# Optimization experiments

Measured on AMD Instinct MI355X. Metric: run time of the kernel, lower is better.

Reference implementation:

```python
import jax, jax.numpy as jnp
import numpy as np

B, N, C, H = 64, 300, 256, 8  # batch, patches (img 1x300, patch 1x1), dim, heads
STD = 0.02


def setup_inputs() -> dict:
    key = jax.random.key(0)
    ks = jax.random.split(key, 6)
    return {
        "x": jax.random.normal(ks[0], (B, N, C), jnp.float32),
        "Wqk": jax.random.normal(ks[1], (2 * C, C), jnp.float32) * STD,
        "Wv": jax.random.normal(ks[2], (C, C), jnp.float32) * STD,
        "Wpos": jax.random.normal(ks[3], (H, 3), jnp.float32) * STD,
        "bpos": jnp.zeros((H,), jnp.float32),
        "Wproj": jax.random.normal(ks[4], (C, C), jnp.float32) * STD,
        "bproj": jnp.zeros((C,), jnp.float32),
        "gating": jnp.ones((H,), jnp.float32),
    }


def _rel_indices(n):
    d = (jnp.arange(n)[None, :] - jnp.arange(n)[:, None]).astype(jnp.float32)
    return jnp.stack([d, jnp.zeros_like(d), d * d], axis=-1)  # [N, N, 3]


def reference(x, Wqk, Wv, Wpos, bpos, Wproj, bproj, gating):
    Bb, Nn, Cc = x.shape
    Hh = gating.shape[0]
    hd = Cc // Hh
    scale = hd ** -0.5

    qk = (x @ Wqk.T).reshape(Bb, Nn, 2, Hh, hd)
    q = qk[:, :, 0].transpose(0, 2, 1, 3)  # [B,H,N,hd]
    k = qk[:, :, 1].transpose(0, 2, 1, 3)

    patch_score = jax.nn.softmax(jnp.einsum('bhnd,bhmd->bhnm', q, k) * scale, axis=-1)

    rel = _rel_indices(Nn)                               # [N,N,3]
    pos_score = (rel @ Wpos.T + bpos).transpose(2, 0, 1)  # [H,N,N]
    pos_score = jax.nn.softmax(pos_score, axis=-1)

    g = jax.nn.sigmoid(gating)[None, :, None, None]       # [1,H,1,1]
    attn = (1.0 - g) * patch_score + g * pos_score[None]
    attn = attn / attn.sum(axis=-1, keepdims=True)

    v = (x @ Wv.T).reshape(Bb, Nn, Hh, hd).transpose(0, 2, 1, 3)  # [B,H,N,hd]
    out = jnp.einsum('bhnm,bhmd->bhnd', attn, v)
    out = out.transpose(0, 2, 1, 3).reshape(Bb, Nn, Cc)
    return out @ Wproj.T + bproj
```

## Files before the change

kernel.cpp:

```cpp
#include <hip/hip_runtime.h>


#define NSEQ 300
#define HEADS 8
#define HD 32

typedef short v8s __attribute__((ext_vector_type(8)));
typedef float v4f __attribute__((ext_vector_type(4)));
typedef unsigned int v4u __attribute__((ext_vector_type(4)));

__device__ __forceinline__ ushort f2bf(float f) {
    unsigned u = __float_as_uint(f);
    u = (u + 0x7FFFu + ((u >> 16) & 1u)) >> 16;
    return (ushort)u;
}

__device__ __forceinline__ unsigned pk2bf(float a, float b) {
    unsigned ua = __float_as_uint(a), ub = __float_as_uint(b);
    ua += 0x7FFFu + ((ua >> 16) & 1u);
    ub += 0x7FFFu + ((ub >> 16) & 1u);
    return __builtin_amdgcn_perm(ub, ua, 0x07060302);
}

__device__ __forceinline__ unsigned cvtpk(float a, float b) {
    unsigned r;
    asm("v_cvt_pk_bf16_f32 %0, %1, %2" : "=v"(r) : "v"(a), "v"(b));
    return r;
}

__device__ __forceinline__ float fexp2(float x) {
    float r; asm("v_exp_f32 %0, %1" : "=v"(r) : "v"(x)); return r;
}

__device__ __forceinline__ void gl_lds16(const ushort* g, ushort* l) {
    __builtin_amdgcn_global_load_lds(
        (const __attribute__((address_space(1))) void*)g,
        (__attribute__((address_space(3))) void*)l, 16, 0, 0);
}

__global__ __launch_bounds__(256) void prep_kernel(
    const float* __restrict__ x,
    const float* __restrict__ Wqk, const float* __restrict__ Wv,
    const float* __restrict__ Wproj, const float* __restrict__ Wpos,
    const float* __restrict__ bpos, const float* __restrict__ gating,
    ushort* __restrict__ x_bf, ushort* __restrict__ Wf,
    ushort* __restrict__ wproj_t, ushort* __restrict__ gpos)
{
    int bid = blockIdx.x, tid = threadIdx.x;
    if (bid < 2432) {
        int idx = bid * 256 + tid;
        int c8 = idx & 31;
        int mrow = idx >> 5;
        unsigned b = (unsigned)mrow / 304u;
        int r = mrow - (int)b * 304;
        v4u pk = {0u, 0u, 0u, 0u};
        if (r < 300) {
            const float* src = x + ((size_t)b * 300 + r) * 256 + c8 * 8;
            float4 f0 = *(const float4*)src;
            float4 f1 = *(const float4*)(src + 4);
            pk = (v4u){pk2bf(f0.x, f0.y), pk2bf(f0.z, f0.w),
                       pk2bf(f1.x, f1.y), pk2bf(f1.z, f1.w)};
        }
        *(v4u*)&x_bf[(size_t)mrow * 256 + c8 * 8] = pk;
        return;
    }
    if (bid < 3040) {
        int sub = bid - 2432;
        int h = sub / 76;
        int i = (sub % 76) * 4 + (tid >> 6);
        int lane = tid & 63;
        ushort* gr = gpos + ((size_t)h * 304 + i) * 304;
        if (i >= NSEQ) {
#pragma unroll
            for (int t = 0; t < 5; ++t) {
                int j = lane + 64 * t;
                if (j < 304) gr[j] = 0;
            }
            return;
        }
        float w0 = Wpos[h * 3 + 0], w2 = Wpos[h * 3 + 2], bb = bpos[h];
        float g = 1.f / (1.f + __expf(-gating[h]));
        float sv[5]; float m2 = -1e30f;
#pragma unroll
        for (int t = 0; t < 5; ++t) {
            int j = lane + 64 * t;
            float d = (float)(j - i);
            float lg = fmaf(w2, d * d, fmaf(w0, d, bb));
            sv[t] = (j < NSEQ) ? lg : -1e30f;
            m2 = fmaxf(m2, sv[t]);
        }
#pragma unroll
        for (int off = 32; off > 0; off >>= 1) m2 = fmaxf(m2, __shfl_xor(m2, off));
        float sum = 0.f;
#pragma unroll
        for (int t = 0; t < 5; ++t) { sv[t] = __expf(sv[t] - m2); sum += sv[t]; }
#pragma unroll
        for (int off = 32; off > 0; off >>= 1) sum += __shfl_xor(sum, off);
        float gi = g / sum;
#pragma unroll
        for (int t = 0; t < 5; ++t) {
            int j = lane + 64 * t;
            if (j < NSEQ) gr[j] = f2bf(sv[t] * gi);
            else if (j < 304) gr[j] = 0;
        }
        return;
    }
    if (bid < 3136) {
        int idx = (bid - 3040) * 256 + tid;
        int c = idx & 7;
        int t = idx >> 3;
        int hk = t / 96;
        int wc = t - hk * 96;
        int h = hk >> 2, kt = hk & 3;
        const float* src;
        if (wc < 32)      src = Wqk + (size_t)(h * 32 + wc) * 256;
        else if (wc < 64) src = Wqk + (size_t)(256 + h * 32 + (wc - 32)) * 256;
        else              src = Wv + (size_t)(h * 32 + (wc - 64)) * 256;
        src += kt * 64 + c * 8;
        float4 f0 = *(const float4*)src;
        float4 f1 = *(const float4*)(src + 4);
        v4u pk = {pk2bf(f0.x, f0.y), pk2bf(f0.z, f0.w),
                  pk2bf(f1.x, f1.y), pk2bf(f1.z, f1.w)};
        *(v4u*)&Wf[((size_t)(hk * 96 + wc)) * 64 + ((c ^ (wc & 7)) * 8)] = pk;
        return;
    }
    {
        int idx = (bid - 3136) * 256 + tid;
        int m = idx >> 5, ck = idx & 31;
        const float* src = Wproj + (size_t)m * 256 + ck * 8;
        int rt = m >> 7, rr = m & 127, kt = ck >> 3, c = ck & 7;
        float4 f0 = *(const float4*)src;
        float4 f1 = *(const float4*)(src + 4);
        v4u pk = {pk2bf(f0.x, f0.y), pk2bf(f0.z, f0.w),
                  pk2bf(f1.x, f1.y), pk2bf(f1.z, f1.w)};
        *(v4u*)&wproj_t[((size_t)(rt * 4 + kt) * 128 + rr) * 64 + ((c ^ (rr & 7)) * 8)] = pk;
    }
}

__global__ __launch_bounds__(256, 2) void fused_qkv_attn(
    const ushort* __restrict__ x_bf, const ushort* __restrict__ Wf,
    const ushort* __restrict__ gpos, const float* __restrict__ gating,
    ushort* __restrict__ ot)
{
    __shared__ ushort smem[34816];
    ushort* Xs = smem;
    ushort* Wsh = smem + 19456;
    ushort* Qs = smem;
    ushort* Ks = smem + 12160;
    ushort* Vt = smem + 24320;

    int bid = blockIdx.x, b = bid & 63, h = bid >> 6;
    int tid = threadIdx.x, wave = tid >> 6, lane = tid & 63, li = lane & 15, qd = lane >> 4;

    const ushort* xbb = x_bf + (size_t)b * 304 * 256;
    const ushort* wfh = Wf + (size_t)h * 4 * 6144;

    v4f acc[5][6];
#pragma unroll
    for (int i = 0; i < 5; ++i)
#pragma unroll
        for (int j = 0; j < 6; ++j) acc[i][j] = (v4f){0.f, 0.f, 0.f, 0.f};

    for (int kt = 0; kt < 4; ++kt) {
#pragma unroll
        for (int s = 0; s < 3; ++s) {
            int c = s * 256 + tid;
            gl_lds16(wfh + (size_t)kt * 6144 + c * 8, Wsh + c * 8);
        }
#pragma unroll
        for (int s = 0; s < 9; ++s) {
            int cch = s * 256 + tid;
            int r = cch >> 3, sl = cch & 7;
            gl_lds16(xbb + (size_t)r * 256 + kt * 64 + ((sl ^ (r & 7)) * 8),
                     Xs + cch * 8);
        }
        if (tid < 128) {
            int cch = 2304 + tid;
            int r = cch >> 3, sl = cch & 7;
            gl_lds16(xbb + (size_t)r * 256 + kt * 64 + ((sl ^ (r & 7)) * 8),
                     Xs + cch * 8);
        }
        __syncthreads();
#pragma unroll
        for (int kc = 0; kc < 64; kc += 32) {
            int cb = (kc >> 3) + qd;
            int cs = cb ^ (li & 7);
            v8s bw[6];
#pragma unroll
            for (int ct = 0; ct < 6; ++ct)
                bw[ct] = *(const v8s*)&Wsh[(ct * 16 + li) * 64 + cs * 8];
#pragma unroll
            for (int i = 0; i < 5; ++i) {
                int rt = wave + i * 4;
                if (rt < 19) {
                    v8s ax = *(const v8s*)&Xs[(rt * 16 + li) * 64 + cs * 8];
#pragma unroll
                    for (int ct = 0; ct < 6; ++ct)
                        acc[i][ct] = __builtin_amdgcn_mfma_f32_16x16x32_bf16(bw[ct], ax, acc[i][ct], 0, 0, 0);
                }
            }
        }
        __syncthreads();
    }

    const float QSC = 0.25503486063f;
#pragma unroll
    for (int i = 0; i < 5; ++i) {
        int rt = wave + i * 4;
        if (rt < 19) {
            int row = rt * 16 + li;
#pragma unroll
            for (int ct = 0; ct < 2; ++ct) {
                uint2 wq = {cvtpk(acc[i][ct][0] * QSC, acc[i][ct][1] * QSC),
                            cvtpk(acc[i][ct][2] * QSC, acc[i][ct][3] * QSC)};
                *(uint2*)&Qs[row * 40 + ct * 16 + qd * 4] = wq;
            }
#pragma unroll
            for (int ct = 2; ct < 4; ++ct) {
                uint2 wk = {cvtpk(acc[i][ct][0], acc[i][ct][1]),
                            cvtpk(acc[i][ct][2], acc[i][ct][3])};
                *(uint2*)&Ks[row * 40 + (ct - 2) * 16 + qd * 4] = wk;
            }
#pragma unroll
            for (int ct = 4; ct < 6; ++ct)
#pragma unroll
                for (int r = 0; r < 4; ++r)
                    Vt[((ct - 4) * 16 + qd * 4 + r) * 328 + row] = f2bf(acc[i][ct][r]);
        }
    }
    float g = 1.f / (1.f + __expf(-gating[h]));
    float omg = 1.f - g;
    __syncthreads();

    const ushort* ksp0 = &Ks[li * 40 + qd * 8];
    const ushort* vtp0 = &Vt[li * 328 + qd * 4];
    const ushort* vtp1 = &Vt[(16 + li) * 328 + qd * 4];
    const v4f z4 = {0.f, 0.f, 0.f, 0.f};

    for (int rg = wave; rg < 19; rg += 4) {
        int i0 = rg * 16;
        v8s bq = *(const v8s*)&Qs[(i0 + li) * 40 + qd * 8];
        const ushort* gp = gpos + ((size_t)h * 304 + (i0 + li)) * 304 + qd * 4;

        v4f Oe0 = z4, Oe1 = z4, Og0 = z4, Og1 = z4;
        float esum = 0.f;

        v8s ak0 = *(const v8s*)(ksp0);
        v8s ak1 = *(const v8s*)(ksp0 + 640);
        uint2 v0a = *(const uint2*)(vtp0);
        uint2 v0b = *(const uint2*)(vtp0 + 16);
        uint2 v1a = *(const uint2*)(vtp1);
        uint2 v1b = *(const uint2*)(vtp1 + 16);
        uint2 gc0 = *(const uint2*)(gp);
        uint2 gc1 = *(const uint2*)(gp + 16);
        uint2 gn0 = *(const uint2*)(gp + 32);
        uint2 gn1 = *(const uint2*)(gp + 48);
        v4f s0n = __builtin_amdgcn_mfma_f32_16x16x32_bf16(ak0, bq, z4, 0, 0, 0);
        v4f s1n = __builtin_amdgcn_mfma_f32_16x16x32_bf16(ak1, bq, z4, 0, 0, 0);

#pragma unroll 1
        for (int p = 0; p < 9; ++p) {
            v4f s0 = s0n, s1 = s1n;
            v8s b0 = __builtin_bit_cast(v8s, (v4u){v0a.x, v0a.y, v0b.x, v0b.y});
            v8s b1 = __builtin_bit_cast(v8s, (v4u){v1a.x, v1a.y, v1b.x, v1b.y});
            v8s ag = __builtin_bit_cast(v8s, (v4u){gc0.x, gc0.y, gc1.x, gc1.y});
            gc0 = gn0; gc1 = gn1;
            int nt0 = 2 * p + 2;
            int nt1 = (p < 8) ? nt0 + 1 : 18;
            int gt0 = (p < 7) ? 2 * p + 4 : 18;
            int gt1 = (p < 7) ? 2 * p + 5 : 18;
            ak0 = *(const v8s*)(ksp0 + nt0 * 640);
            ak1 = *(const v8s*)(ksp0 + nt1 * 640);
            v0a = *(const uint2*)(vtp0 + nt0 * 16);
            v0b = *(const uint2*)(vtp0 + nt1 * 16);
            v1a = *(const uint2*)(vtp1 + nt0 * 16);
            v1b = *(const uint2*)(vtp1 + nt1 * 16);
            gn0 = *(const uint2*)(gp + gt0 * 16);
            gn1 = *(const uint2*)(gp + gt1 * 16);
            s0n = __builtin_amdgcn_mfma_f32_16x16x32_bf16(ak0, bq, z4, 0, 0, 0);
            s1n = __builtin_amdgcn_mfma_f32_16x16x32_bf16(ak1, bq, z4, 0, 0, 0);

            float e0 = fexp2(s0[0]);
            float e1 = fexp2(s0[1]);
            float e2 = fexp2(s0[2]);
            float e3 = fexp2(s0[3]);
            float f0 = fexp2(s1[0]);
            float f1 = fexp2(s1[1]);
            float f2 = fexp2(s1[2]);
            float f3 = fexp2(s1[3]);
            esum += ((e0 + e1) + (e2 + e3)) + ((f0 + f1) + (f2 + f3));
            v8s ae = __builtin_bit_cast(v8s, (v4u){cvtpk(e0, e1), cvtpk(e2, e3),
                                                   cvtpk(f0, f1), cvtpk(f2, f3)});
            __builtin_amdgcn_s_setprio(1);
            Oe0 = __builtin_amdgcn_mfma_f32_16x16x32_bf16(ae, b0, Oe0, 0, 0, 0);
            Oe1 = __builtin_amdgcn_mfma_f32_16x16x32_bf16(ae, b1, Oe1, 0, 0, 0);
            Og0 = __builtin_amdgcn_mfma_f32_16x16x32_bf16(ag, b0, Og0, 0, 0, 0);
            Og1 = __builtin_amdgcn_mfma_f32_16x16x32_bf16(ag, b1, Og1, 0, 0, 0);
            __builtin_amdgcn_s_setprio(0);
        }
        {
            float e0 = fexp2(s0n[0]);
            float e1 = fexp2(s0n[1]);
            float e2 = fexp2(s0n[2]);
            float e3 = fexp2(s0n[3]);
            if (qd == 3) { e0 = e1 = e2 = e3 = 0.f; }
            esum += (e0 + e1) + (e2 + e3);
            v8s ae = __builtin_bit_cast(v8s, (v4u){cvtpk(e0, e1), cvtpk(e2, e3), 0u, 0u});
            v8s ag = __builtin_bit_cast(v8s, (v4u){gc0.x, gc0.y, 0u, 0u});
            v8s b0 = __builtin_bit_cast(v8s, (v4u){v0a.x, v0a.y, 0u, 0u});
            v8s b1 = __builtin_bit_cast(v8s, (v4u){v1a.x, v1a.y, 0u, 0u});
            Oe0 = __builtin_amdgcn_mfma_f32_16x16x32_bf16(ae, b0, Oe0, 0, 0, 0);
            Oe1 = __builtin_amdgcn_mfma_f32_16x16x32_bf16(ae, b1, Oe1, 0, 0, 0);
            Og0 = __builtin_amdgcn_mfma_f32_16x16x32_bf16(ag, b0, Og0, 0, 0, 0);
            Og1 = __builtin_amdgcn_mfma_f32_16x16x32_bf16(ag, b1, Og1, 0, 0, 0);
        }
        esum += __shfl_xor(esum, 16);
        esum += __shfl_xor(esum, 32);
        float ps = omg / esum;
        float psr[4];
#pragma unroll
        for (int r = 0; r < 4; ++r) psr[r] = __shfl(ps, qd * 4 + r);
#pragma unroll
        for (int r = 0; r < 4; ++r) {
            int row = i0 + qd * 4 + r;
            if (row < NSEQ) {
                int m = b * NSEQ + row;
                int rt = m >> 7, rr = m & 127;
                int c0 = (h & 1) * 4 + (li >> 3);
                int p2 = li & 7;
                size_t tb = ((size_t)(rt * 4 + (h >> 1)) * 128 + rr) * 64;
                ot[tb + ((c0 ^ (rr & 7)) * 8) + p2] = f2bf(fmaf(psr[r], Oe0[r], Og0[r]));
                ot[tb + (((c0 + 2) ^ (rr & 7)) * 8) + p2] = f2bf(fmaf(psr[r], Oe1[r], Og1[r]));
            }
        }
    }
}

__global__ __launch_bounds__(256, 4) void gemm_proj_mfma(
    const ushort* __restrict__ A, const ushort* __restrict__ Bw,
    const float* __restrict__ bias, float* __restrict__ out)
{
    __shared__ ushort As[64 * 64];
    __shared__ ushort Bs[128 * 64];
    int tid = threadIdx.x;
    int wave = tid >> 6, lane = tid & 63, li = lane & 15, qd = lane >> 4;
    int rh = wave >> 1, ch = wave & 1;
    int by = blockIdx.y;
    const ushort* gA = A + ((size_t)(by >> 1) * 4 * 128 + (by & 1) * 64) * 64;
    const ushort* gB = Bw + (size_t)blockIdx.x * 4 * 8192;

    v4f acc[2][4];
#pragma unroll
    for (int i = 0; i < 2; ++i)
#pragma unroll
        for (int j = 0; j < 4; ++j) acc[i][j] = (v4f){0.f, 0.f, 0.f, 0.f};

    for (int kt = 0; kt < 4; ++kt) {
#pragma unroll
        for (int s = 0; s < 2; ++s) {
            int cch = s * 256 + tid;
            gl_lds16(gA + (size_t)kt * 128 * 64 + cch * 8, As + cch * 8);
        }
#pragma unroll
        for (int s = 0; s < 4; ++s) {
            int cch = s * 256 + tid;
            gl_lds16(gB + (size_t)kt * 8192 + cch * 8, Bs + cch * 8);
        }
        __syncthreads();
#pragma unroll
        for (int kc = 0; kc < 64; kc += 32) {
            int cb = (kc >> 3) + qd;
            int cs = cb ^ (li & 7);
            v8s a[2], b[4];
#pragma unroll
            for (int mt = 0; mt < 2; ++mt)
                a[mt] = *(const v8s*)&As[(rh * 32 + mt * 16 + li) * 64 + cs * 8];
#pragma unroll
            for (int nt = 0; nt < 4; ++nt)
                b[nt] = *(const v8s*)&Bs[(ch * 64 + nt * 16 + li) * 64 + cs * 8];
#pragma unroll
            for (int mt = 0; mt < 2; ++mt)
#pragma unroll
                for (int nt = 0; nt < 4; ++nt)
                    acc[mt][nt] = __builtin_amdgcn_mfma_f32_16x16x32_bf16(b[nt], a[mt], acc[mt][nt], 0, 0, 0);
        }
        __syncthreads();
    }

#pragma unroll
    for (int mt = 0; mt < 2; ++mt) {
        int row = by * 64 + rh * 32 + mt * 16 + li;
#pragma unroll
        for (int nt = 0; nt < 4; ++nt) {
            int col = blockIdx.x * 128 + ch * 64 + nt * 16 + qd * 4;
            float4 bv = *(const float4*)&bias[col];
            float4 st = {acc[mt][nt][0] + bv.x, acc[mt][nt][1] + bv.y,
                         acc[mt][nt][2] + bv.z, acc[mt][nt][3] + bv.w};
            *(float4*)&out[(size_t)row * 256 + col] = st;
        }
    }
}

extern "C" void kernel_launch(void* const* d_in, const int* in_sizes, int n_in,
                              void* d_out, int out_size, void* d_ws, size_t ws_size,
                              hipStream_t stream) {
    const float* x      = (const float*)d_in[0];
    const float* Wqk    = (const float*)d_in[1];
    const float* Wv     = (const float*)d_in[2];
    const float* Wpos   = (const float*)d_in[3];
    const float* bpos   = (const float*)d_in[4];
    const float* Wproj  = (const float*)d_in[5];
    const float* bproj  = (const float*)d_in[6];
    const float* gating = (const float*)d_in[7];
    float* out = (float*)d_out;

    ushort* gpos     = (ushort*)d_ws;
    ushort* Wf       = gpos + 739328;
    ushort* wproj_t  = Wf + 196608;
    ushort* o_t      = wproj_t + 65536;
    ushort* x_bf     = o_t + 4915200;

    prep_kernel<<<3168, 256, 0, stream>>>(x, Wqk, Wv, Wproj, Wpos, bpos, gating,
                                          x_bf, Wf, wproj_t, gpos);
    fused_qkv_attn<<<512, 256, 0, stream>>>(x_bf, Wf, gpos, gating, o_t);
    gemm_proj_mfma<<<dim3(2, 300), 256, 0, stream>>>(o_t, wproj_t, bproj, out);
}
```

Measured before the change: 124.8 us.

## Use 512-thread blocks and keep Q in registers via shuffles in fused attention

Doubles the fused QKV+attention block to 8 waves, so each wave owns fewer 16-row tiles (3 instead of 5) and needs fewer accumulators. Q is no longer staged in LDS: the MFMA output fragments are rearranged with lane shuffles into the operand layout and carried in registers across row-group iterations. This shrinks shared memory and register use, allowing more waves per CU for latency hiding. The cost is extra shuffle work, and the wider waves leave some idle, since 19 row tiles do not divide evenly across 8 waves.

```diff
diff --git a/kernel.cpp b/kernel.cpp
--- a/kernel.cpp
+++ b/kernel.cpp
@@ -137,17 +137,16 @@
     }
 }
 
-__global__ __launch_bounds__(256, 2) void fused_qkv_attn(
+__global__ __launch_bounds__(512, 4) void fused_qkv_attn(
     const ushort* __restrict__ x_bf, const ushort* __restrict__ Wf,
     const ushort* __restrict__ gpos, const float* __restrict__ gating,
     ushort* __restrict__ ot)
 {
-    __shared__ ushort smem[34816];
+    __shared__ ushort smem[25600];
     ushort* Xs = smem;
     ushort* Wsh = smem + 19456;
-    ushort* Qs = smem;
-    ushort* Ks = smem + 12160;
-    ushort* Vt = smem + 24320;
+    ushort* Ks = smem;
+    ushort* Vt = smem + 12160;
 
     int bid = blockIdx.x, b = bid & 63, h = bid >> 6;
     int tid = threadIdx.x, wave = tid >> 6, lane = tid & 63, li = lane & 15, qd = lane >> 4;
@@ -155,27 +154,25 @@
     const ushort* xbb = x_bf + (size_t)b * 304 * 256;
     const ushort* wfh = Wf + (size_t)h * 4 * 6144;
 
-    v4f acc[5][6];
-#pragma unroll
-    for (int i = 0; i < 5; ++i)
+    v4f acc[3][6];
+#pragma unroll
+    for (int i = 0; i < 3; ++i)
 #pragma unroll
         for (int j = 0; j < 6; ++j) acc[i][j] = (v4f){0.f, 0.f, 0.f, 0.f};
 
     for (int kt = 0; kt < 4; ++kt) {
-#pragma unroll
-        for (int s = 0; s < 3; ++s) {
-            int c = s * 256 + tid;
-            gl_lds16(wfh + (size_t)kt * 6144 + c * 8, Wsh + c * 8);
-        }
-#pragma unroll
-        for (int s = 0; s < 9; ++s) {
-            int cch = s * 256 + tid;
+        gl_lds16(wfh + (size_t)kt * 6144 + tid * 8, Wsh + tid * 8);
+        if (tid < 256)
+            gl_lds16(wfh + (size_t)kt * 6144 + (512 + tid) * 8, Wsh + (512 + tid) * 8);
+#pragma unroll
+        for (int s = 0; s < 4; ++s) {
+            int cch = s * 512 + tid;
             int r = cch >> 3, sl = cch & 7;
             gl_lds16(xbb + (size_t)r * 256 + kt * 64 + ((sl ^ (r & 7)) * 8),
                      Xs + cch * 8);
         }
-        if (tid < 128) {
-            int cch = 2304 + tid;
+        if (tid < 384) {
+            int cch = 2048 + tid;
             int r = cch >> 3, sl = cch & 7;
             gl_lds16(xbb + (size_t)r * 256 + kt * 64 + ((sl ^ (r & 7)) * 8),
                      Xs + cch * 8);
@@ -190,8 +187,8 @@
             for (int ct = 0; ct < 6; ++ct)
                 bw[ct] = *(const v8s*)&Wsh[(ct * 16 + li) * 64 + cs * 8];
 #pragma unroll
-            for (int i = 0; i < 5; ++i) {
-                int rt = wave + i * 4;
+            for (int i = 0; i < 3; ++i) {
+                int rt = wave + i * 8;
                 if (rt < 19) {
                     v8s ax = *(const v8s*)&Xs[(rt * 16 + li) * 64 + cs * 8];
 #pragma unroll
@@ -204,17 +201,26 @@
     }
 
     const float QSC = 0.25503486063f;
-#pragma unroll
-    for (int i = 0; i < 5; ++i) {
-        int rt = wave + i * 4;
+    v4u q0 = {0,0,0,0}, q1 = {0,0,0,0}, q2 = {0,0,0,0};
+    int srcA = ((qd & 1) << 5) + li;
+    int srcB = srcA + 16;
+#pragma unroll
+    for (int i = 0; i < 3; ++i) {
+        int rt = wave + i * 8;
         if (rt < 19) {
+            unsigned W00 = cvtpk(acc[i][0][0] * QSC, acc[i][0][1] * QSC);
+            unsigned W01 = cvtpk(acc[i][0][2] * QSC, acc[i][0][3] * QSC);
+            unsigned W10 = cvtpk(acc[i][1][0] * QSC, acc[i][1][1] * QSC);
+            unsigned W11 = cvtpk(acc[i][1][2] * QSC, acc[i][1][3] * QSC);
+            unsigned a0 = __shfl(W00, srcA), a1 = __shfl(W01, srcA);
+            unsigned a2 = __shfl(W00, srcB), a3 = __shfl(W01, srcB);
+            unsigned b0 = __shfl(W10, srcA), b1 = __shfl(W11, srcA);
+            unsigned b2 = __shfl(W10, srcB), b3 = __shfl(W11, srcB);
+            bool hi = (qd >= 2);
+            v4u qq = {hi ? b0 : a0, hi ? b1 : a1, hi ? b2 : a2, hi ? b3 : a3};
+            if (i == 0) q0 = qq; else if (i == 1) q1 = qq; else q2 = qq;
+
             int row = rt * 16 + li;
-#pragma unroll
-            for (int ct = 0; ct < 2; ++ct) {
-                uint2 wq = {cvtpk(acc[i][ct][0] * QSC, acc[i][ct][1] * QSC),
-                            cvtpk(acc[i][ct][2] * QSC, acc[i][ct][3] * QSC)};
-                *(uint2*)&Qs[row * 40 + ct * 16 + qd * 4] = wq;
-            }
 #pragma unroll
             for (int ct = 2; ct < 4; ++ct) {
                 uint2 wk = {cvtpk(acc[i][ct][0], acc[i][ct][1]),
@@ -237,9 +243,10 @@
     const ushort* vtp1 = &Vt[(16 + li) * 328 + qd * 4];
     const v4f z4 = {0.f, 0.f, 0.f, 0.f};
 
-    for (int rg = wave; rg < 19; rg += 4) {
+#pragma unroll 1
+    for (int rg = wave; rg < 19; rg += 8) {
         int i0 = rg * 16;
-        v8s bq = *(const v8s*)&Qs[(i0 + li) * 40 + qd * 8];
+        v8s bq = __builtin_bit_cast(v8s, q0);
         const ushort* gp = gpos + ((size_t)h * 304 + (i0 + li)) * 304 + qd * 4;
 
         v4f Oe0 = z4, Oe1 = z4, Og0 = z4, Og1 = z4;
@@ -333,6 +340,7 @@
                 ot[tb + (((c0 + 2) ^ (rr & 7)) * 8) + p2] = f2bf(fmaf(psr[r], Oe1[r], Og1[r]));
             }
         }
+        q0 = q1; q1 = q2;
     }
 }
 
@@ -422,6 +430,6 @@
 
     prep_kernel<<<3168, 256, 0, stream>>>(x, Wqk, Wv, Wproj, Wpos, bpos, gating,
                                           x_bf, Wf, wproj_t, gpos);
-    fused_qkv_attn<<<512, 256, 0, stream>>>(x_bf, Wf, gpos, gating, o_t);
+    fused_qkv_attn<<<512, 512, 0, stream>>>(x_bf, Wf, gpos, gating, o_t);
     gemm_proj_mfma<<<dim3(2, 300), 256, 0, stream>>>(o_t, wproj_t, bproj, out);
 }
```

Result: no change. 122.9 us (-1.5%).
